# Kernel tuning notes

Hardware: AMD Instinct MI355X
Metric: run time of the kernel (lower is better)

Reference implementation:

```python
import jax, jax.numpy as jnp
import numpy as np

VOCAB, E, H, L, N = 32000, 256, 512, 512, 64


def setup_inputs() -> dict:
    key = jax.random.key(0)
    ks = jax.random.split(key, 8)
    s_in = 1.0 / np.sqrt(H + E)
    return {
        "x": jax.random.randint(ks[0], (L, N), 0, VOCAB),
        "emb": jax.random.normal(ks[1], (VOCAB, E), dtype=jnp.float32),
        # weights stored (in, out); math identical to torch Linear with W.T
        "Wz": jax.random.uniform(ks[2], (H + E, H), jnp.float32, -s_in, s_in),
        "bz": jax.random.uniform(ks[3], (H,), jnp.float32, -s_in, s_in),
        "Wr": jax.random.uniform(ks[4], (H + E, H), jnp.float32, -s_in, s_in),
        "br": jax.random.uniform(ks[5], (H,), jnp.float32, -s_in, s_in),
        "Wh": jax.random.uniform(ks[6], (H + E, H), jnp.float32, -s_in, s_in),
        "bh": jax.random.uniform(ks[7], (H,), jnp.float32, -s_in, s_in),
    }


def reference(x, emb, Wz, bz, Wr, br, Wh, bh):
    # x: (L, N) int indices -> embedded once: (L, N, E)
    xe = emb[x]
    h0 = jnp.zeros((x.shape[1], Wz.shape[1]), dtype=emb.dtype)

    def step(h, e_t):
        hx = jnp.concatenate([h, e_t], axis=1)            # (N, H+E)
        z = jax.nn.sigmoid(hx @ Wz + bz)                  # update gate
        r = jax.nn.sigmoid(hx @ Wr + br)                  # reset gate
        rhx = jnp.concatenate([r * h, e_t], axis=1)
        h_tilde = jnp.tanh(rhx @ Wh + bh)
        h_new = (1.0 - z) * h + z * h_tilde
        return h_new, h_new

    _, hs = jax.lax.scan(step, h0, xe)                    # hs: (L, N, H)
    return hs
```

## Files before the change

kernel.cpp:

```cpp
#include <hip/hip_runtime.h>


#define LSTEPS 512
#define NBATCH 64
#define HDIM   512
#define EDIM   256
#define KDIM   768
#define NBLK   32
#define TPB    256

typedef _Float16 f16x8 __attribute__((ext_vector_type(8)));
typedef float    f32x4 __attribute__((ext_vector_type(4)));

__device__ __forceinline__ float sigm(float x){ return 1.0f/(1.0f+__expf(-x)); }
__device__ __forceinline__ float tanh_fast(float x){
  float e = __expf(2.0f*x);
  return 1.0f - 2.0f/(e + 1.0f);
}
__device__ __forceinline__ unsigned f16b(float x){
  union { _Float16 h; unsigned short u; } c; c.h = (_Float16)x; return (unsigned)c.u;
}

__global__ void prep_w(const float* __restrict__ Wz, const float* __restrict__ Wr,
                       const float* __restrict__ Wh, _Float16* __restrict__ wbuf){
  int tid = blockIdx.x*256 + threadIdx.x;
  int g   = tid / (HDIM*KDIM);
  int rem = tid - g*(HDIM*KDIM);
  int j   = rem / KDIM;
  int k   = rem - j*KDIM;
  const float* W = (g==0) ? Wz : ((g==1) ? Wr : Wh);
  wbuf[tid] = (_Float16)W[(size_t)k*HDIM + j];
}

__global__ void prep_emb(const int* __restrict__ x, const float* __restrict__ emb,
                         _Float16* __restrict__ ebuf){
  int tid = blockIdx.x*256 + threadIdx.x;
  int k4  = tid & 63;
  int tn  = tid >> 6;
  int row = x[tn];
  const float4 v = *(const float4*)(emb + (size_t)row*EDIM + (k4<<2));
  union { _Float16 h[4]; uint2 u; } p;
  p.h[0] = (_Float16)v.x; p.h[1] = (_Float16)v.y;
  p.h[2] = (_Float16)v.z; p.h[3] = (_Float16)v.w;
  *(uint2*)(ebuf + (size_t)tn*EDIM + (k4<<2)) = p.u;
}

__device__ __forceinline__ void wait_flags(unsigned* flags, unsigned target){
  const int l = threadIdx.x & 63;
  for (;;){
    unsigned v = target;
    if (l < NBLK) v = __hip_atomic_load(&flags[l], __ATOMIC_RELAXED, __HIP_MEMORY_SCOPE_AGENT);
    if (__all(v >= target)) break;
  }
  __builtin_amdgcn_fence(__ATOMIC_ACQUIRE, "agent");
}

__device__ __forceinline__ void store_x(_Float16* buf, int jc2, int n0, int lane,
                                        float v0, float v1, float v2, float v3){
  unsigned p01 = f16b(v0) | (f16b(v1) << 16);
  unsigned p23 = f16b(v2) | (f16b(v3) << 16);
  unsigned q01 = __shfl_xor(p01, 1, 64);
  unsigned q23 = __shfl_xor(p23, 1, 64);
  unsigned w0, w1; int r0;
  if (lane & 1){
    w0 = (q23 & 0xffffu) | (p23 << 16);
    w1 = (q23 >> 16)     | (p23 & 0xffff0000u);
    r0 = n0 + 2;
  } else {
    w0 = (p01 & 0xffffu) | (q01 << 16);
    w1 = (p01 >> 16)     | (q01 & 0xffff0000u);
    r0 = n0;
  }
  __hip_atomic_store((unsigned*)(buf + (size_t)r0*HDIM + jc2),     w0,
                     __ATOMIC_RELAXED, __HIP_MEMORY_SCOPE_AGENT);
  __hip_atomic_store((unsigned*)(buf + (size_t)(r0+1)*HDIM + jc2), w1,
                     __ATOMIC_RELAXED, __HIP_MEMORY_SCOPE_AGENT);
}

__global__ __launch_bounds__(TPB) void gru_persist(
    const _Float16* __restrict__ wbuf,
    const _Float16* __restrict__ ebuf,
    const float* __restrict__ bz, const float* __restrict__ br, const float* __restrict__ bh,
    _Float16* __restrict__ hbuf,
    _Float16* __restrict__ rhbuf,
    float* __restrict__ out,
    unsigned* __restrict__ flags)
{
  __shared__ char wlds[3*16*1536];
  const int jbase = blockIdx.x * 16;

  for (int cidx = threadIdx.x; cidx < 3*16*96; cidx += TPB){
    int g   = cidx / (16*96);
    int rem = cidx - g*(16*96);
    int col = rem / 96;
    int kch = rem - col*96;
    const uint4 v = *(const uint4*)(wbuf + ((size_t)(g*HDIM + jbase + col))*KDIM + kch*8);
    int off = (((g*16 + col)*1536) + kch*16) ^ ((col & 7) << 4);
    *(uint4*)(wlds + off) = v;
  }
  __syncthreads();

  const int lane = threadIdx.x & 63;
  const int wave = threadIdx.x >> 6;
  const int c15  = lane & 15;
  const int kgrp = lane >> 4;
  const int jcol = jbase + c15;
  const int jc2  = jcol & ~1;
  const int arow = wave*16 + c15;
  const int n0   = wave*16 + kgrp*4;
  const int swz  = (c15 & 7) << 4;
  const int linz = ((      c15)*1536) + kgrp*16;
  const int linr = ((16  + c15)*1536) + kgrp*16;
  const int linh = ((32  + c15)*1536) + kgrp*16;
  const float bzj = bz[jcol];
  const float brj = br[jcol];
  const float bhj = bh[jcol];
  float hreg[4] = {0.f, 0.f, 0.f, 0.f};

  unsigned gen = 0;
  for (int t = 0; t < LSTEPS; ++t){
    const _Float16* et = ebuf + (size_t)t*(NBATCH*EDIM);
    const _Float16* ae = et + arow*EDIM + kgrp*8;

    f32x4 accz = {0.f,0.f,0.f,0.f};
    f32x4 accr = {0.f,0.f,0.f,0.f};
    #pragma unroll
    for (int kc = 0; kc < 8; ++kc){
      f16x8 a   = *(const f16x8*)(ae + kc*32);
      f16x8 bzv = *(const f16x8*)(wlds + ((linz + (16+kc)*64) ^ swz));
      f16x8 brv = *(const f16x8*)(wlds + ((linr + (16+kc)*64) ^ swz));
      accz = __builtin_amdgcn_mfma_f32_16x16x32_f16(a, bzv, accz, 0, 0, 0);
      accr = __builtin_amdgcn_mfma_f32_16x16x32_f16(a, brv, accr, 0, 0, 0);
    }
    wait_flags(flags, gen);
    {
      const _Float16* ah = hbuf + arow*HDIM + kgrp*8;
      #pragma unroll
      for (int kc = 0; kc < 16; ++kc){
        f16x8 a   = *(const f16x8*)(ah + kc*32);
        f16x8 bzv = *(const f16x8*)(wlds + ((linz + kc*64) ^ swz));
        f16x8 brv = *(const f16x8*)(wlds + ((linr + kc*64) ^ swz));
        accz = __builtin_amdgcn_mfma_f32_16x16x32_f16(a, bzv, accz, 0, 0, 0);
        accr = __builtin_amdgcn_mfma_f32_16x16x32_f16(a, brv, accr, 0, 0, 0);
      }
    }
    float zreg[4], rh[4];
    #pragma unroll
    for (int i = 0; i < 4; ++i){
      zreg[i] = sigm(accz[i] + bzj);
      rh[i]   = sigm(accr[i] + brj) * hreg[i];
    }
    store_x(rhbuf, jc2, n0, lane, rh[0], rh[1], rh[2], rh[3]);
    __syncthreads();
    if (threadIdx.x == 0)
      __hip_atomic_store(&flags[blockIdx.x], gen+1,
                         __ATOMIC_RELEASE, __HIP_MEMORY_SCOPE_AGENT);

    f32x4 acch = {0.f,0.f,0.f,0.f};
    #pragma unroll
    for (int kc = 0; kc < 8; ++kc){
      f16x8 a   = *(const f16x8*)(ae + kc*32);
      f16x8 bhv = *(const f16x8*)(wlds + ((linh + (16+kc)*64) ^ swz));
      acch = __builtin_amdgcn_mfma_f32_16x16x32_f16(a, bhv, acch, 0, 0, 0);
    }
    wait_flags(flags, gen+1);
    {
      const _Float16* ar = rhbuf + arow*HDIM + kgrp*8;
      #pragma unroll
      for (int kc = 0; kc < 16; ++kc){
        f16x8 a   = *(const f16x8*)(ar + kc*32);
        f16x8 bhv = *(const f16x8*)(wlds + ((linh + kc*64) ^ swz));
        acch = __builtin_amdgcn_mfma_f32_16x16x32_f16(a, bhv, acch, 0, 0, 0);
      }
    }
    #pragma unroll
    for (int i = 0; i < 4; ++i){
      float ht = tanh_fast(acch[i] + bhj);
      float hn = hreg[i] + zreg[i]*(ht - hreg[i]);
      hreg[i] = hn;
      out[((size_t)t*NBATCH + (n0+i))*HDIM + jcol] = hn;
    }
    store_x(hbuf, jc2, n0, lane, hreg[0], hreg[1], hreg[2], hreg[3]);
    __syncthreads();
    if (threadIdx.x == 0)
      __hip_atomic_store(&flags[blockIdx.x], gen+2,
                         __ATOMIC_RELEASE, __HIP_MEMORY_SCOPE_AGENT);
    gen += 2;
  }
}

extern "C" void kernel_launch(void* const* d_in, const int* in_sizes, int n_in,
                              void* d_out, int out_size, void* d_ws, size_t ws_size,
                              hipStream_t stream) {
  const int*   x   = (const int*)  d_in[0];
  const float* emb = (const float*)d_in[1];
  const float* Wz  = (const float*)d_in[2];
  const float* bz  = (const float*)d_in[3];
  const float* Wr  = (const float*)d_in[4];
  const float* br  = (const float*)d_in[5];
  const float* Wh  = (const float*)d_in[6];
  const float* bh  = (const float*)d_in[7];
  float* out = (float*)d_out;
  char*  ws  = (char*)d_ws;

  size_t off = 0;
  unsigned*  flags = (unsigned*)(ws + off); off += 256;
  _Float16*  hbuf  = (_Float16*)(ws + off); off += (size_t)NBATCH*HDIM*2;
  size_t zero_bytes = off;
  _Float16*  rhbuf = (_Float16*)(ws + off); off += (size_t)NBATCH*HDIM*2;
  _Float16*  wbuf  = (_Float16*)(ws + off); off += (size_t)3*HDIM*KDIM*2;
  _Float16*  ebuf  = (_Float16*)(ws + off); off += (size_t)LSTEPS*NBATCH*EDIM*2;

  hipMemsetAsync(ws, 0, zero_bytes, stream);

  prep_w  <<<(3*HDIM*KDIM)/256,          256, 0, stream>>>(Wz, Wr, Wh, wbuf);
  prep_emb<<<(LSTEPS*NBATCH*EDIM/4)/256, 256, 0, stream>>>(x, emb, ebuf);
  gru_persist<<<NBLK, TPB, 0, stream>>>(wbuf, ebuf, bz, br, bh,
                                        hbuf, rhbuf, out, flags);
}
```

Measured before the change: 5.934 ms.

## Replace flag barriers with step-tagged 64-bit hidden-state words

Each f16 pair of h and r*h is now stored alongside its timestep tag in a single 64-bit atomic word. Consumers spin until every word they loaded carries the expected tag, then use the data directly. This drops the per-phase __syncthreads, the flag store and the separate flag polling, so one memory round trip per handoff goes away. In exchange it doubles the bytes written and polled for the state, and holds 64 u64 values in registers, which raises VGPR pressure.

```diff
diff --git a/kernel.cpp b/kernel.cpp
--- a/kernel.cpp
+++ b/kernel.cpp
@@ -11,6 +11,7 @@
 
 typedef _Float16 f16x8 __attribute__((ext_vector_type(8)));
 typedef float    f32x4 __attribute__((ext_vector_type(4)));
+typedef unsigned long long u64;
 
 __device__ __forceinline__ float sigm(float x){ return 1.0f/(1.0f+__expf(-x)); }
 __device__ __forceinline__ float tanh_fast(float x){
@@ -45,18 +46,9 @@
   *(uint2*)(ebuf + (size_t)tn*EDIM + (k4<<2)) = p.u;
 }
 
-__device__ __forceinline__ void wait_flags(unsigned* flags, unsigned target){
-  const int l = threadIdx.x & 63;
-  for (;;){
-    unsigned v = target;
-    if (l < NBLK) v = __hip_atomic_load(&flags[l], __ATOMIC_RELAXED, __HIP_MEMORY_SCOPE_AGENT);
-    if (__all(v >= target)) break;
-  }
-  __builtin_amdgcn_fence(__ATOMIC_ACQUIRE, "agent");
-}
-
-__device__ __forceinline__ void store_x(_Float16* buf, int jc2, int n0, int lane,
-                                        float v0, float v1, float v2, float v3){
+__device__ __forceinline__ void store_tagged(u64* buf, int jc2u, int n0, int lane,
+                                             unsigned tag,
+                                             float v0, float v1, float v2, float v3){
   unsigned p01 = f16b(v0) | (f16b(v1) << 16);
   unsigned p23 = f16b(v2) | (f16b(v3) << 16);
   unsigned q01 = __shfl_xor(p01, 1, 64);
@@ -71,20 +63,20 @@
     w1 = (p01 >> 16)     | (q01 & 0xffff0000u);
     r0 = n0;
   }
-  __hip_atomic_store((unsigned*)(buf + (size_t)r0*HDIM + jc2),     w0,
+  u64 t64 = ((u64)tag) << 32;
+  __hip_atomic_store(buf + (size_t)r0*256 + jc2u,     t64 | (u64)w0,
                      __ATOMIC_RELAXED, __HIP_MEMORY_SCOPE_AGENT);
-  __hip_atomic_store((unsigned*)(buf + (size_t)(r0+1)*HDIM + jc2), w1,
+  __hip_atomic_store(buf + (size_t)(r0+1)*256 + jc2u, t64 | (u64)w1,
                      __ATOMIC_RELAXED, __HIP_MEMORY_SCOPE_AGENT);
 }
 
-__global__ __launch_bounds__(TPB) void gru_persist(
+__global__ __launch_bounds__(TPB, 1) void gru_persist(
     const _Float16* __restrict__ wbuf,
     const _Float16* __restrict__ ebuf,
     const float* __restrict__ bz, const float* __restrict__ br, const float* __restrict__ bh,
-    _Float16* __restrict__ hbuf,
-    _Float16* __restrict__ rhbuf,
-    float* __restrict__ out,
-    unsigned* __restrict__ flags)
+    u64* __restrict__ hx,
+    u64* __restrict__ rhx,
+    float* __restrict__ out)
 {
   __shared__ char wlds[3*16*1536];
   const int jbase = blockIdx.x * 16;
@@ -105,7 +97,7 @@
   const int c15  = lane & 15;
   const int kgrp = lane >> 4;
   const int jcol = jbase + c15;
-  const int jc2  = jcol & ~1;
+  const int jc2u = jcol >> 1;
   const int arow = wave*16 + c15;
   const int n0   = wave*16 + kgrp*4;
   const int swz  = (c15 & 7) << 4;
@@ -115,13 +107,28 @@
   const float bzj = bz[jcol];
   const float brj = br[jcol];
   const float bhj = bh[jcol];
+  const u64* hrow  = hx  + (size_t)arow*256 + kgrp*4;
+  const u64* rhrow = rhx + (size_t)arow*256 + kgrp*4;
   float hreg[4] = {0.f, 0.f, 0.f, 0.f};
 
-  unsigned gen = 0;
+  u64 q[64];
+
+#define LOADQ(BASE) do {                                                      \
+    _Pragma("unroll")                                                         \
+    for (int kc = 0; kc < 16; ++kc){                                          \
+      _Pragma("unroll")                                                       \
+      for (int i = 0; i < 4; ++i)                                             \
+        q[kc*4+i] = __hip_atomic_load((BASE) + kc*16 + i,                     \
+                      __ATOMIC_RELAXED, __HIP_MEMORY_SCOPE_AGENT);            \
+    }                                                                         \
+  } while (0)
+
   for (int t = 0; t < LSTEPS; ++t){
-    const _Float16* et = ebuf + (size_t)t*(NBATCH*EDIM);
-    const _Float16* ae = et + arow*EDIM + kgrp*8;
-
+    const _Float16* ae = ebuf + ((size_t)t*NBATCH + arow)*EDIM + kgrp*8;
+    const unsigned texp = (unsigned)t;
+    const unsigned twr  = (unsigned)(t + 1);
+
+    LOADQ(hrow);
     f32x4 accz = {0.f,0.f,0.f,0.f};
     f32x4 accr = {0.f,0.f,0.f,0.f};
     #pragma unroll
@@ -132,17 +139,22 @@
       accz = __builtin_amdgcn_mfma_f32_16x16x32_f16(a, bzv, accz, 0, 0, 0);
       accr = __builtin_amdgcn_mfma_f32_16x16x32_f16(a, brv, accr, 0, 0, 0);
     }
-    wait_flags(flags, gen);
-    {
-      const _Float16* ah = hbuf + arow*HDIM + kgrp*8;
-      #pragma unroll
-      for (int kc = 0; kc < 16; ++kc){
-        f16x8 a   = *(const f16x8*)(ah + kc*32);
-        f16x8 bzv = *(const f16x8*)(wlds + ((linz + kc*64) ^ swz));
-        f16x8 brv = *(const f16x8*)(wlds + ((linr + kc*64) ^ swz));
-        accz = __builtin_amdgcn_mfma_f32_16x16x32_f16(a, bzv, accz, 0, 0, 0);
-        accr = __builtin_amdgcn_mfma_f32_16x16x32_f16(a, brv, accr, 0, 0, 0);
-      }
+    for (;;){
+      unsigned err = 0;
+      #pragma unroll
+      for (int i = 0; i < 64; ++i) err |= ((unsigned)(q[i] >> 32)) ^ texp;
+      if (!__any(err != 0)) break;
+      LOADQ(hrow);
+    }
+    #pragma unroll
+    for (int kc = 0; kc < 16; ++kc){
+      union { unsigned u[4]; f16x8 v; } a;
+      #pragma unroll
+      for (int i = 0; i < 4; ++i) a.u[i] = (unsigned)q[kc*4+i];
+      f16x8 bzv = *(const f16x8*)(wlds + ((linz + kc*64) ^ swz));
+      f16x8 brv = *(const f16x8*)(wlds + ((linr + kc*64) ^ swz));
+      accz = __builtin_amdgcn_mfma_f32_16x16x32_f16(a.v, bzv, accz, 0, 0, 0);
+      accr = __builtin_amdgcn_mfma_f32_16x16x32_f16(a.v, brv, accr, 0, 0, 0);
     }
     float zreg[4], rh[4];
     #pragma unroll
@@ -150,12 +162,9 @@
       zreg[i] = sigm(accz[i] + bzj);
       rh[i]   = sigm(accr[i] + brj) * hreg[i];
     }
-    store_x(rhbuf, jc2, n0, lane, rh[0], rh[1], rh[2], rh[3]);
-    __syncthreads();
-    if (threadIdx.x == 0)
-      __hip_atomic_store(&flags[blockIdx.x], gen+1,
-                         __ATOMIC_RELEASE, __HIP_MEMORY_SCOPE_AGENT);
-
+    store_tagged(rhx, jc2u, n0, lane, twr, rh[0], rh[1], rh[2], rh[3]);
+
+    LOADQ(rhrow);
     f32x4 acch = {0.f,0.f,0.f,0.f};
     #pragma unroll
     for (int kc = 0; kc < 8; ++kc){
@@ -163,15 +172,20 @@
       f16x8 bhv = *(const f16x8*)(wlds + ((linh + (16+kc)*64) ^ swz));
       acch = __builtin_amdgcn_mfma_f32_16x16x32_f16(a, bhv, acch, 0, 0, 0);
     }
-    wait_flags(flags, gen+1);
-    {
-      const _Float16* ar = rhbuf + arow*HDIM + kgrp*8;
-      #pragma unroll
-      for (int kc = 0; kc < 16; ++kc){
-        f16x8 a   = *(const f16x8*)(ar + kc*32);
-        f16x8 bhv = *(const f16x8*)(wlds + ((linh + kc*64) ^ swz));
-        acch = __builtin_amdgcn_mfma_f32_16x16x32_f16(a, bhv, acch, 0, 0, 0);
-      }
+    for (;;){
+      unsigned err = 0;
+      #pragma unroll
+      for (int i = 0; i < 64; ++i) err |= ((unsigned)(q[i] >> 32)) ^ twr;
+      if (!__any(err != 0)) break;
+      LOADQ(rhrow);
+    }
+    #pragma unroll
+    for (int kc = 0; kc < 16; ++kc){
+      union { unsigned u[4]; f16x8 v; } a;
+      #pragma unroll
+      for (int i = 0; i < 4; ++i) a.u[i] = (unsigned)q[kc*4+i];
+      f16x8 bhv = *(const f16x8*)(wlds + ((linh + kc*64) ^ swz));
+      acch = __builtin_amdgcn_mfma_f32_16x16x32_f16(a.v, bhv, acch, 0, 0, 0);
     }
     #pragma unroll
     for (int i = 0; i < 4; ++i){
@@ -180,13 +194,9 @@
       hreg[i] = hn;
       out[((size_t)t*NBATCH + (n0+i))*HDIM + jcol] = hn;
     }
-    store_x(hbuf, jc2, n0, lane, hreg[0], hreg[1], hreg[2], hreg[3]);
-    __syncthreads();
-    if (threadIdx.x == 0)
-      __hip_atomic_store(&flags[blockIdx.x], gen+2,
-                         __ATOMIC_RELEASE, __HIP_MEMORY_SCOPE_AGENT);
-    gen += 2;
+    store_tagged(hx, jc2u, n0, lane, twr, hreg[0], hreg[1], hreg[2], hreg[3]);
   }
+#undef LOADQ
 }
 
 extern "C" void kernel_launch(void* const* d_in, const int* in_sizes, int n_in,
@@ -204,17 +214,15 @@
   char*  ws  = (char*)d_ws;
 
   size_t off = 0;
-  unsigned*  flags = (unsigned*)(ws + off); off += 256;
-  _Float16*  hbuf  = (_Float16*)(ws + off); off += (size_t)NBATCH*HDIM*2;
+  u64* hx  = (u64*)(ws + off); off += (size_t)NBATCH*(HDIM/2)*8;
+  u64* rhx = (u64*)(ws + off); off += (size_t)NBATCH*(HDIM/2)*8;
   size_t zero_bytes = off;
-  _Float16*  rhbuf = (_Float16*)(ws + off); off += (size_t)NBATCH*HDIM*2;
-  _Float16*  wbuf  = (_Float16*)(ws + off); off += (size_t)3*HDIM*KDIM*2;
-  _Float16*  ebuf  = (_Float16*)(ws + off); off += (size_t)LSTEPS*NBATCH*EDIM*2;
+  _Float16* wbuf = (_Float16*)(ws + off); off += (size_t)3*HDIM*KDIM*2;
+  _Float16* ebuf = (_Float16*)(ws + off); off += (size_t)LSTEPS*NBATCH*EDIM*2;
 
   hipMemsetAsync(ws, 0, zero_bytes, stream);
 
   prep_w  <<<(3*HDIM*KDIM)/256,          256, 0, stream>>>(Wz, Wr, Wh, wbuf);
   prep_emb<<<(LSTEPS*NBATCH*EDIM/4)/256, 256, 0, stream>>>(x, emb, ebuf);
-  gru_persist<<<NBLK, TPB, 0, stream>>>(wbuf, ebuf, bz, br, bh,
-                                        hbuf, rhbuf, out, flags);
-}
+  gru_persist<<<NBLK, TPB, 0, stream>>>(wbuf, ebuf, bz, br, bh, hx, rhx, out);
+}
```

Result: slower. 15.44 ms (+160.2%).
